# Performance work log

Hardware: AMD Instinct MI355X
Metric: run time of the kernel (lower is better)

Reference implementation:

```python
import jax, jax.numpy as jnp
import numpy as np

N_NODES = 50000
N_EDGES = 800000
IN_DIM, HID_DIM, OUT_DIM = 128, 64, 64


def spmm(row, col, val, dense):
    # sparse [N,N] (COO) @ dense [N,D] -> [N,D]
    gathered = dense[col] * val[:, None]          # [E, D]
    return jax.ops.segment_sum(gathered, row, num_segments=N_NODES)


def setup_inputs() -> dict:
    key = jax.random.key(0)
    ks = jax.random.split(key, 8)
    stdv1 = 1.0 / np.sqrt(HID_DIM)
    stdv2 = 1.0 / np.sqrt(OUT_DIM)
    return {
        "x": jax.random.normal(ks[0], (N_NODES, IN_DIM), dtype=jnp.float32),
        "edge_row": jax.random.randint(ks[1], (N_EDGES,), 0, N_NODES, dtype=jnp.int32),
        "edge_col": jax.random.randint(ks[2], (N_EDGES,), 0, N_NODES, dtype=jnp.int32),
        "edge_val": jax.random.uniform(ks[3], (N_EDGES,), dtype=jnp.float32),
        "W1": jax.random.uniform(ks[4], (IN_DIM, HID_DIM), jnp.float32, -stdv1, stdv1),
        "b1": jax.random.uniform(ks[5], (HID_DIM,), jnp.float32, -stdv1, stdv1),
        "W2": jax.random.uniform(ks[6], (HID_DIM, OUT_DIM), jnp.float32, -stdv2, stdv2),
        "b2": jax.random.uniform(ks[7], (OUT_DIM,), jnp.float32, -stdv2, stdv2),
    }


def reference(x, edge_row, edge_col, edge_val, W1, b1, W2, b2):
    # layer 1: support = x @ W1; out = adj @ support + b1; relu
    h = jax.nn.relu(spmm(edge_row, edge_col, edge_val, x @ W1) + b1)
    # dropout: eval mode (training=False) -> identity
    # layer 2
    return spmm(edge_row, edge_col, edge_val, h @ W2) + b2
```

## Files before the change

### kernel.cpp

```cpp
#include <hip/hip_runtime.h>


#define N_NODES 50000
#define N_EDGES 800000
#define IN_DIM  128
#define HID_DIM 64
#define OUT_DIM 64

#define RB   256
#define NB   ((N_NODES + RB - 1) / RB)
#define EPB  1024
#define NBLK_E ((N_EDGES + EPB - 1) / EPB)
#define BCAP 5120
#define GEMM_GRID ((N_NODES + 31) / 32)

typedef __attribute__((ext_vector_type(8))) short bf16x8;
typedef __attribute__((ext_vector_type(4))) float f32x4;

__device__ inline unsigned short f2bf(float x) {
    unsigned u = __float_as_uint(x);
    return (unsigned short)((u + 0x7FFFu + ((u >> 16) & 1u)) >> 16);
}
__device__ inline float bf2f(unsigned v) {
    return __uint_as_float(v << 16);
}

__global__ __launch_bounds__(256) void k_prep(
    const float* __restrict__ W1, unsigned short* __restrict__ Wt1,
    const float* __restrict__ W2, unsigned short* __restrict__ Wt2,
    int* __restrict__ bcur)
{
    int b = blockIdx.x, t = threadIdx.x;
    if (b < 32) {
        int e = b * 256 + t;
        int c = e / IN_DIM, k = e % IN_DIM;
        Wt1[c * IN_DIM + k] = f2bf(W1[k * HID_DIM + c]);
    } else if (b < 48) {
        int e2 = (b - 32) * 256 + t;
        int c = e2 / HID_DIM, k = e2 % HID_DIM;
        Wt2[c * HID_DIM + k] = f2bf(W2[k * OUT_DIM + c]);
    } else {
        if (t < NB) bcur[t] = 0;
    }
}

__global__ __launch_bounds__(256) void k_bscatter(
    const int* __restrict__ erow, const int* __restrict__ ecol,
    const float* __restrict__ eval_, int* __restrict__ bcur,
    uint2* __restrict__ bucketed)
{
    __shared__ uint2 sbuf[EPB];
    __shared__ int lc[NB];
    __shared__ int scr[256];
    __shared__ int lbase[NB];
    int t = threadIdx.x;
    if (t < NB) lc[t] = 0;
    __syncthreads();
    int base = blockIdx.x * EPB;
    int ne = min(EPB, N_EDGES - base);
    int bkt[4], rnk[4];
    unsigned w0v[4], vv[4];
    #pragma unroll
    for (int i = 0; i < 4; ++i) {
        int e = base + i * 256 + t;
        bkt[i] = -1;
        if (e < N_EDGES) {
            unsigned r = (unsigned)erow[e];
            bkt[i] = (int)(r >> 8);
            w0v[i] = (unsigned)ecol[e] | ((r & 255u) << 16) | ((r >> 8) << 24);
            vv[i] = __float_as_uint(eval_[e]);
            rnk[i] = atomicAdd(&lc[bkt[i]], 1);
        }
    }
    __syncthreads();
    int cnt = (t < NB) ? lc[t] : 0;
    scr[t] = cnt;
    __syncthreads();
    #pragma unroll
    for (int off = 1; off < 256; off <<= 1) {
        int add = (t >= off) ? scr[t - off] : 0;
        __syncthreads();
        scr[t] += add;
        __syncthreads();
    }
    int excl = scr[t] - cnt;
    __syncthreads();
    scr[t] = excl;
    if (t < NB) lbase[t] = cnt ? atomicAdd(&bcur[t], cnt) : 0;
    __syncthreads();
    #pragma unroll
    for (int i = 0; i < 4; ++i)
        if (bkt[i] >= 0)
            sbuf[scr[bkt[i]] + rnk[i]] = make_uint2(w0v[i], vv[i]);
    __syncthreads();
    #pragma unroll
    for (int i = 0; i < 4; ++i) {
        int idx = i * 256 + t;
        if (idx < ne) {
            uint2 p = sbuf[idx];
            int bk = (int)(p.x >> 24);
            bucketed[(size_t)bk * BCAP + lbase[bk] + (idx - scr[bk])] = p;
        }
    }
}

__global__ __launch_bounds__(256) void k_bfinal(
    const int* __restrict__ bcur, const uint2* __restrict__ bucketed,
    uint2* __restrict__ pairs, int2* __restrict__ offs2)
{
    __shared__ uint2 ebuf[BCAP];
    __shared__ int rcnt[256];
    __shared__ int rsc[256];
    int t = threadIdx.x, b = blockIdx.x;
    int ne = bcur[b];
    int base0 = b * BCAP;
    rcnt[t] = 0;
    __syncthreads();
    for (int i = t; i < ne; i += 256) {
        uint2 p = bucketed[(size_t)base0 + i];
        ebuf[i] = p;
        atomicAdd(&rcnt[(p.x >> 16) & 255], 1);
    }
    __syncthreads();
    int v = rcnt[t];
    rsc[t] = v;
    __syncthreads();
    #pragma unroll
    for (int off = 1; off < 256; off <<= 1) {
        int add = (t >= off) ? rsc[t - off] : 0;
        __syncthreads();
        rsc[t] += add;
        __syncthreads();
    }
    int start = base0 + rsc[t] - v;
    int gr = (b << 8) + t;
    if (gr < N_NODES) offs2[gr] = make_int2(start, start + v);
    rcnt[t] = start;
    __syncthreads();
    for (int i = t; i < ne; i += 256) {
        uint2 p = ebuf[i];
        int pos = atomicAdd(&rcnt[(p.x >> 16) & 255], 1);
        pairs[pos] = make_uint2(p.x & 0xFFFFu, p.y);
    }
}

template <int K, bool IN_BF16>
__device__ __forceinline__ void gemm_body(
    unsigned short* __restrict__ Al, unsigned short* __restrict__ Bl,
    const void* __restrict__ Xv, const unsigned short* __restrict__ Wt,
    unsigned short* __restrict__ out, int bid, int t)
{
    int m0 = bid * 32;
    #pragma unroll
    for (int i = 0; i < K / 32; ++i) {
        int u4 = i * 256 + t;
        int col = (u4 * 8) / K, k = (u4 * 8) % K;
        uint4 w = ((const uint4*)Wt)[u4];
        int byte = (col * K + k) * 2;
        byte ^= ((col & 7) << 4);
        *(uint4*)((char*)Bl + byte) = w;
    }
    if (IN_BF16) {
        const unsigned short* X = (const unsigned short*)Xv;
        int row = t / (K / 8), k = (t % (K / 8)) * 8;
        int grow = m0 + row;
        uint4 v = make_uint4(0, 0, 0, 0);
        if (grow < N_NODES)
            v = *(const uint4*)(X + (size_t)grow * K + k);
        int byte = (row * K + k) * 2;
        byte ^= ((row & 7) << 4);
        *(uint4*)((char*)Al + byte) = v;
    } else {
        const float* X = (const float*)Xv;
        #pragma unroll
        for (int i = 0; i < K / 64; ++i) {
            int f8 = i * 256 + t;
            int row = (f8 * 8) / K, k = (f8 * 8) % K;
            int grow = m0 + row;
            float4 xa = make_float4(0.f, 0.f, 0.f, 0.f), xb = xa;
            if (grow < N_NODES) {
                const float4* src = (const float4*)(X + (size_t)grow * K + k);
                xa = src[0];
                xb = src[1];
            }
            uint4 v;
            v.x = (unsigned)f2bf(xa.x) | ((unsigned)f2bf(xa.y) << 16);
            v.y = (unsigned)f2bf(xa.z) | ((unsigned)f2bf(xa.w) << 16);
            v.z = (unsigned)f2bf(xb.x) | ((unsigned)f2bf(xb.y) << 16);
            v.w = (unsigned)f2bf(xb.z) | ((unsigned)f2bf(xb.w) << 16);
            int byte = (row * K + k) * 2;
            byte ^= ((row & 7) << 4);
            *(uint4*)((char*)Al + byte) = v;
        }
    }
    __syncthreads();

    int w = t >> 6, l = t & 63;
    int lr0 = (w & 1) * 16;
    int c0  = (w >> 1) * 32;
    int lrow = lr0 + (l & 15);
    int kb = (l >> 4) * 8;
    int col0 = c0 + (l & 15), col1 = col0 + 16;
    f32x4 acc0 = {0.f, 0.f, 0.f, 0.f}, acc1 = {0.f, 0.f, 0.f, 0.f};
    #pragma unroll
    for (int kc = 0; kc < K / 32; ++kc) {
        int ka = kc * 32 + kb;
        int ab = (lrow * K + ka) * 2;  ab ^= ((lrow & 7) << 4);
        int bb0 = (col0 * K + ka) * 2; bb0 ^= ((col0 & 7) << 4);
        int bb1 = (col1 * K + ka) * 2; bb1 ^= ((col1 & 7) << 4);
        bf16x8 a  = *(const bf16x8*)((const char*)Al + ab);
        bf16x8 b0 = *(const bf16x8*)((const char*)Bl + bb0);
        bf16x8 b1 = *(const bf16x8*)((const char*)Bl + bb1);
        acc0 = __builtin_amdgcn_mfma_f32_16x16x32_bf16(a, b0, acc0, 0, 0, 0);
        acc1 = __builtin_amdgcn_mfma_f32_16x16x32_bf16(a, b1, acc1, 0, 0, 0);
    }
    int grow0 = m0 + lr0 + (l >> 4) * 4;
    #pragma unroll
    for (int j = 0; j < 4; ++j) {
        int gr = grow0 + j;
        if (gr < N_NODES) {
            out[(size_t)gr * 64 + col0] = f2bf(acc0[j]);
            out[(size_t)gr * 64 + col1] = f2bf(acc1[j]);
        }
    }
}

__global__ __launch_bounds__(256) void k_gemm1(
    const float* __restrict__ X, const unsigned short* __restrict__ Wt,
    unsigned short* __restrict__ out)
{
    __shared__ unsigned short Al[32 * IN_DIM];
    __shared__ unsigned short Bl[64 * IN_DIM];
    gemm_body<IN_DIM, false>(Al, Bl, X, Wt, out, blockIdx.x, threadIdx.x);
}

__global__ __launch_bounds__(512) void k_gather_gemm1(
    const int2* __restrict__ offs2, const uint2* __restrict__ pairs,
    const unsigned short* __restrict__ dense, const float* __restrict__ b1,
    const unsigned short* __restrict__ Wt2, unsigned short* __restrict__ out)
{
    __shared__ unsigned short Al[32 * 64];
    __shared__ unsigned short Bl[64 * 64];
    int t = threadIdx.x;
    int m0 = blockIdx.x * 32;
    {
        int u4 = t;
        int col = (u4 * 8) / 64, k = (u4 * 8) % 64;
        uint4 wv = ((const uint4*)Wt2)[u4];
        int byte = (col * 64 + k) * 2;
        byte ^= ((col & 7) << 4);
        *(uint4*)((char*)Bl + byte) = wv;
    }
    int w = t >> 6, d = t & 63;
    #pragma unroll 1
    for (int j = 0; j < 4; ++j) {
        int lr = w * 4 + j;
        int r = __builtin_amdgcn_readfirstlane(m0 + lr);
        float acc = 0.f;
        if (r < N_NODES) {
            int2 oe = offs2[r];
            int e0 = oe.x, e1 = oe.y;
            float a[8];
            a[0] = b1[d];
            #pragma unroll
            for (int i = 1; i < 8; ++i) a[i] = 0.f;
            int e = e0;
            for (; e + 8 <= e1; e += 8) {
                uint2 p[8];
                #pragma unroll
                for (int i = 0; i < 8; ++i) p[i] = pairs[e + i];
                unsigned v[8];
                #pragma unroll
                for (int i = 0; i < 8; ++i) v[i] = dense[(size_t)p[i].x * 64u + d];
                #pragma unroll
                for (int i = 0; i < 8; ++i)
                    a[i] = fmaf(__uint_as_float(p[i].y), bf2f(v[i]), a[i]);
            }
            if (e + 4 <= e1) {
                uint2 p[4];
                #pragma unroll
                for (int i = 0; i < 4; ++i) p[i] = pairs[e + i];
                unsigned v[4];
                #pragma unroll
                for (int i = 0; i < 4; ++i) v[i] = dense[(size_t)p[i].x * 64u + d];
                #pragma unroll
                for (int i = 0; i < 4; ++i)
                    a[i] = fmaf(__uint_as_float(p[i].y), bf2f(v[i]), a[i]);
                e += 4;
            }
            for (; e < e1; ++e) {
                uint2 p = pairs[e];
                a[0] = fmaf(__uint_as_float(p.y),
                            bf2f(dense[(size_t)p.x * 64u + d]), a[0]);
            }
            acc = ((a[0] + a[1]) + (a[2] + a[3])) +
                  ((a[4] + a[5]) + (a[6] + a[7]));
            acc = fmaxf(acc, 0.f);
        }
        int byte = (lr * 64 + d) * 2;
        byte ^= ((lr & 7) << 4);
        *(unsigned short*)((char*)Al + byte) = f2bf(acc);
    }
    __syncthreads();
    int l = t & 63;
    int lr0 = (w & 1) * 16;
    int c0  = (w >> 1) * 16;
    int lrow = lr0 + (l & 15);
    int kb = (l >> 4) * 8;
    int col = c0 + (l & 15);
    f32x4 acc0 = {0.f, 0.f, 0.f, 0.f};
    #pragma unroll
    for (int kc = 0; kc < 2; ++kc) {
        int ka = kc * 32 + kb;
        int ab = (lrow * 64 + ka) * 2; ab ^= ((lrow & 7) << 4);
        int bb = (col * 64 + ka) * 2;  bb ^= ((col & 7) << 4);
        bf16x8 a = *(const bf16x8*)((const char*)Al + ab);
        bf16x8 b = *(const bf16x8*)((const char*)Bl + bb);
        acc0 = __builtin_amdgcn_mfma_f32_16x16x32_bf16(a, b, acc0, 0, 0, 0);
    }
    int grow0 = m0 + lr0 + (l >> 4) * 4;
    #pragma unroll
    for (int j = 0; j < 4; ++j) {
        int gr = grow0 + j;
        if (gr < N_NODES)
            out[(size_t)gr * 64 + col] = f2bf(acc0[j]);
    }
}

__global__ __launch_bounds__(256) void k_gather2(
    const int2* __restrict__ offs2, const uint2* __restrict__ pairs,
    const unsigned short* __restrict__ dense, const float* __restrict__ bias,
    float* __restrict__ outp)
{
    int t = threadIdx.x;
    int r = __builtin_amdgcn_readfirstlane(blockIdx.x * 4 + (t >> 6));
    int d = t & 63;
    int2 oe = offs2[r];
    int e0 = oe.x, e1 = oe.y;
    float a[8];
    a[0] = bias[d];
    #pragma unroll
    for (int i = 1; i < 8; ++i) a[i] = 0.f;
    int e = e0;
    for (; e + 8 <= e1; e += 8) {
        uint2 p[8];
        #pragma unroll
        for (int i = 0; i < 8; ++i) p[i] = pairs[e + i];
        unsigned v[8];
        #pragma unroll
        for (int i = 0; i < 8; ++i) v[i] = dense[(size_t)p[i].x * 64u + d];
        #pragma unroll
        for (int i = 0; i < 8; ++i)
            a[i] = fmaf(__uint_as_float(p[i].y), bf2f(v[i]), a[i]);
    }
    if (e + 4 <= e1) {
        uint2 p[4];
        #pragma unroll
        for (int i = 0; i < 4; ++i) p[i] = pairs[e + i];
        unsigned v[4];
        #pragma unroll
        for (int i = 0; i < 4; ++i) v[i] = dense[(size_t)p[i].x * 64u + d];
        #pragma unroll
        for (int i = 0; i < 4; ++i)
            a[i] = fmaf(__uint_as_float(p[i].y), bf2f(v[i]), a[i]);
        e += 4;
    }
    for (; e < e1; ++e) {
        uint2 p = pairs[e];
        a[0] = fmaf(__uint_as_float(p.y),
                    bf2f(dense[(size_t)p.x * 64u + d]), a[0]);
    }
    float acc = ((a[0] + a[1]) + (a[2] + a[3])) +
                ((a[4] + a[5]) + (a[6] + a[7]));
    outp[(size_t)r * 64 + d] = acc;
}

extern "C" void kernel_launch(void* const* d_in, const int* in_sizes, int n_in,
                              void* d_out, int out_size, void* d_ws, size_t ws_size,
                              hipStream_t stream)
{
    const float* x     = (const float*)d_in[0];
    const int*   erow  = (const int*)d_in[1];
    const int*   ecol  = (const int*)d_in[2];
    const float* eval_ = (const float*)d_in[3];
    const float* W1    = (const float*)d_in[4];
    const float* b1    = (const float*)d_in[5];
    const float* W2    = (const float*)d_in[6];
    const float* b2    = (const float*)d_in[7];
    float* out = (float*)d_out;

    uint2* pairs    = (uint2*)d_ws;
    uint2* bucketed = pairs + (size_t)NB * BCAP;
    unsigned short* support = (unsigned short*)(bucketed + (size_t)NB * BCAP);
    unsigned short* Wt1 = support + (size_t)N_NODES * 64;
    unsigned short* Wt2 = Wt1 + IN_DIM * HID_DIM;
    int*  bcur  = (int*)(Wt2 + HID_DIM * OUT_DIM);
    int2* offs2 = (int2*)(bcur + NB);

    unsigned short* support2 = (unsigned short*)(offs2 + N_NODES + 2);

    const int row_grid = N_NODES / 4;

    k_prep<<<49, 256, 0, stream>>>(W1, Wt1, W2, Wt2, bcur);
    k_bscatter<<<NBLK_E, 256, 0, stream>>>(erow, ecol, eval_, bcur, bucketed);
    k_bfinal<<<NB, 256, 0, stream>>>(bcur, bucketed, pairs, offs2);
    k_gemm1<<<GEMM_GRID, 256, 0, stream>>>(x, Wt1, support);
    k_gather_gemm1<<<GEMM_GRID, 512, 0, stream>>>(
        offs2, pairs, support, b1, Wt2, support2);
    k_gather2<<<row_grid, 256, 0, stream>>>(
        offs2, pairs, support2, b2, out);
}
```

Before: 96.68 us.

## Fuse bucket scatter with first GEMM, split bucket finalize, deepen gather unroll

Bucket scatter and the x@W1 GEMM now run as one launch, with block ranges assigned to each role and a shared LDS buffer, so the two independent stages overlap and one launch disappears. Bucket finalization is split into two blocks per bucket, each handling half the rows with a wave-level shuffle scan. It rereads the bucket from global memory instead of staging it in a 40KB LDS buffer, which should raise occupancy and parallelism at the cost of a second read. The layer-2 gather is unrolled to 16 edges per iteration for more memory-level parallelism, which raises register use.

```diff
diff --git a/kernel.cpp b/kernel.cpp
--- a/kernel.cpp
+++ b/kernel.cpp
@@ -41,106 +41,6 @@
         Wt2[c * HID_DIM + k] = f2bf(W2[k * OUT_DIM + c]);
     } else {
         if (t < NB) bcur[t] = 0;
-    }
-}
-
-__global__ __launch_bounds__(256) void k_bscatter(
-    const int* __restrict__ erow, const int* __restrict__ ecol,
-    const float* __restrict__ eval_, int* __restrict__ bcur,
-    uint2* __restrict__ bucketed)
-{
-    __shared__ uint2 sbuf[EPB];
-    __shared__ int lc[NB];
-    __shared__ int scr[256];
-    __shared__ int lbase[NB];
-    int t = threadIdx.x;
-    if (t < NB) lc[t] = 0;
-    __syncthreads();
-    int base = blockIdx.x * EPB;
-    int ne = min(EPB, N_EDGES - base);
-    int bkt[4], rnk[4];
-    unsigned w0v[4], vv[4];
-    #pragma unroll
-    for (int i = 0; i < 4; ++i) {
-        int e = base + i * 256 + t;
-        bkt[i] = -1;
-        if (e < N_EDGES) {
-            unsigned r = (unsigned)erow[e];
-            bkt[i] = (int)(r >> 8);
-            w0v[i] = (unsigned)ecol[e] | ((r & 255u) << 16) | ((r >> 8) << 24);
-            vv[i] = __float_as_uint(eval_[e]);
-            rnk[i] = atomicAdd(&lc[bkt[i]], 1);
-        }
-    }
-    __syncthreads();
-    int cnt = (t < NB) ? lc[t] : 0;
-    scr[t] = cnt;
-    __syncthreads();
-    #pragma unroll
-    for (int off = 1; off < 256; off <<= 1) {
-        int add = (t >= off) ? scr[t - off] : 0;
-        __syncthreads();
-        scr[t] += add;
-        __syncthreads();
-    }
-    int excl = scr[t] - cnt;
-    __syncthreads();
-    scr[t] = excl;
-    if (t < NB) lbase[t] = cnt ? atomicAdd(&bcur[t], cnt) : 0;
-    __syncthreads();
-    #pragma unroll
-    for (int i = 0; i < 4; ++i)
-        if (bkt[i] >= 0)
-            sbuf[scr[bkt[i]] + rnk[i]] = make_uint2(w0v[i], vv[i]);
-    __syncthreads();
-    #pragma unroll
-    for (int i = 0; i < 4; ++i) {
-        int idx = i * 256 + t;
-        if (idx < ne) {
-            uint2 p = sbuf[idx];
-            int bk = (int)(p.x >> 24);
-            bucketed[(size_t)bk * BCAP + lbase[bk] + (idx - scr[bk])] = p;
-        }
-    }
-}
-
-__global__ __launch_bounds__(256) void k_bfinal(
-    const int* __restrict__ bcur, const uint2* __restrict__ bucketed,
-    uint2* __restrict__ pairs, int2* __restrict__ offs2)
-{
-    __shared__ uint2 ebuf[BCAP];
-    __shared__ int rcnt[256];
-    __shared__ int rsc[256];
-    int t = threadIdx.x, b = blockIdx.x;
-    int ne = bcur[b];
-    int base0 = b * BCAP;
-    rcnt[t] = 0;
-    __syncthreads();
-    for (int i = t; i < ne; i += 256) {
-        uint2 p = bucketed[(size_t)base0 + i];
-        ebuf[i] = p;
-        atomicAdd(&rcnt[(p.x >> 16) & 255], 1);
-    }
-    __syncthreads();
-    int v = rcnt[t];
-    rsc[t] = v;
-    __syncthreads();
-    #pragma unroll
-    for (int off = 1; off < 256; off <<= 1) {
-        int add = (t >= off) ? rsc[t - off] : 0;
-        __syncthreads();
-        rsc[t] += add;
-        __syncthreads();
-    }
-    int start = base0 + rsc[t] - v;
-    int gr = (b << 8) + t;
-    if (gr < N_NODES) offs2[gr] = make_int2(start, start + v);
-    rcnt[t] = start;
-    __syncthreads();
-    for (int i = t; i < ne; i += 256) {
-        uint2 p = ebuf[i];
-        int pos = atomicAdd(&rcnt[(p.x >> 16) & 255], 1);
-        pairs[pos] = make_uint2(p.x & 0xFFFFu, p.y);
     }
 }
 
@@ -225,13 +125,125 @@
     }
 }
 
-__global__ __launch_bounds__(256) void k_gemm1(
-    const float* __restrict__ X, const unsigned short* __restrict__ Wt,
-    unsigned short* __restrict__ out)
-{
-    __shared__ unsigned short Al[32 * IN_DIM];
-    __shared__ unsigned short Bl[64 * IN_DIM];
-    gemm_body<IN_DIM, false>(Al, Bl, X, Wt, out, blockIdx.x, threadIdx.x);
+__global__ __launch_bounds__(256) void k_mega(
+    const int* __restrict__ erow, const int* __restrict__ ecol,
+    const float* __restrict__ eval_, int* __restrict__ bcur,
+    uint2* __restrict__ bucketed,
+    const float* __restrict__ X, const unsigned short* __restrict__ Wt1,
+    unsigned short* __restrict__ support)
+{
+    __shared__ __align__(16) unsigned char smem[24576];
+    int t = threadIdx.x;
+    if (blockIdx.x >= NBLK_E) {
+        gemm_body<IN_DIM, false>((unsigned short*)smem,
+                                 (unsigned short*)(smem + 8192),
+                                 X, Wt1, support, blockIdx.x - NBLK_E, t);
+        return;
+    }
+    uint2* sbuf  = (uint2*)smem;
+    int*   lc    = (int*)(smem + 8192);
+    int*   scr   = lc + 256;
+    int*   lbase = scr + 256;
+    if (t < NB) lc[t] = 0;
+    __syncthreads();
+    int base = blockIdx.x * EPB;
+    int ne = min(EPB, N_EDGES - base);
+    int bkt[4], rnk[4];
+    unsigned w0v[4], vv[4];
+    #pragma unroll
+    for (int i = 0; i < 4; ++i) {
+        int e = base + i * 256 + t;
+        bkt[i] = -1;
+        if (e < N_EDGES) {
+            unsigned r = (unsigned)erow[e];
+            bkt[i] = (int)(r >> 8);
+            w0v[i] = (unsigned)ecol[e] | ((r & 255u) << 16) | ((r >> 8) << 24);
+            vv[i] = __float_as_uint(eval_[e]);
+            rnk[i] = atomicAdd(&lc[bkt[i]], 1);
+        }
+    }
+    __syncthreads();
+    int cnt = (t < NB) ? lc[t] : 0;
+    scr[t] = cnt;
+    __syncthreads();
+    #pragma unroll
+    for (int off = 1; off < 256; off <<= 1) {
+        int add = (t >= off) ? scr[t - off] : 0;
+        __syncthreads();
+        scr[t] += add;
+        __syncthreads();
+    }
+    int excl = scr[t] - cnt;
+    __syncthreads();
+    scr[t] = excl;
+    if (t < NB) lbase[t] = cnt ? atomicAdd(&bcur[t], cnt) : 0;
+    __syncthreads();
+    #pragma unroll
+    for (int i = 0; i < 4; ++i)
+        if (bkt[i] >= 0)
+            sbuf[scr[bkt[i]] + rnk[i]] = make_uint2(w0v[i], vv[i]);
+    __syncthreads();
+    #pragma unroll
+    for (int i = 0; i < 4; ++i) {
+        int idx = i * 256 + t;
+        if (idx < ne) {
+            uint2 p = sbuf[idx];
+            int bk = (int)(p.x >> 24);
+            bucketed[(size_t)bk * BCAP + lbase[bk] + (idx - scr[bk])] = p;
+        }
+    }
+}
+
+__global__ __launch_bounds__(256) void k_bfinal2(
+    const int* __restrict__ bcur, const uint2* __restrict__ bucketed,
+    uint2* __restrict__ pairs, int2* __restrict__ offs2)
+{
+    __shared__ int rcnt[128], rst[128];
+    __shared__ int nkept_sh;
+    int t = threadIdx.x, blk = blockIdx.x;
+    int B = blk >> 1, h = blk & 1;
+    int ne = bcur[B];
+    size_t eb = (size_t)B * BCAP;
+    if (t < 128) rcnt[t] = 0;
+    __syncthreads();
+    for (int i = t; i < ne; i += 256) {
+        unsigned w0 = bucketed[eb + i].x;
+        int rl = (int)((w0 >> 16) & 255u);
+        if ((rl >> 7) == h) atomicAdd(&rcnt[rl & 127], 1);
+    }
+    __syncthreads();
+    if (t < 64) {
+        int c0 = rcnt[2 * t], c1 = rcnt[2 * t + 1];
+        int s = c0 + c1, inc = s;
+        #pragma unroll
+        for (int off = 1; off < 64; off <<= 1) {
+            int o = __shfl_up(inc, off, 64);
+            if (t >= off) inc += o;
+        }
+        int excl = inc - s;
+        int tot = __shfl(inc, 63, 64);
+        if (t == 0) nkept_sh = tot;
+        rst[2 * t] = excl;
+        rst[2 * t + 1] = excl + c0;
+    }
+    __syncthreads();
+    int nk = nkept_sh;
+    int regionBase = (int)eb + (h ? (ne - nk) : 0);
+    if (t < 128) {
+        int gr = B * 256 + h * 128 + t;
+        int st = regionBase + rst[t];
+        if (gr < N_NODES) offs2[gr] = make_int2(st, st + rcnt[t]);
+        rst[t] = st;
+    }
+    __syncthreads();
+    for (int i = t; i < ne; i += 256) {
+        uint2 p = bucketed[eb + i];
+        int rl = (int)((p.x >> 16) & 255u);
+        if ((rl >> 7) == h) {
+            int pos = atomicAdd(&rst[rl & 127], 1);
+            pairs[pos] = make_uint2(p.x & 0xFFFFu, p.y);
+        }
+    }
 }
 
 __global__ __launch_bounds__(512) void k_gather_gemm1(
@@ -337,12 +349,23 @@
     int d = t & 63;
     int2 oe = offs2[r];
     int e0 = oe.x, e1 = oe.y;
-    float a[8];
+    float a[16];
     a[0] = bias[d];
     #pragma unroll
-    for (int i = 1; i < 8; ++i) a[i] = 0.f;
+    for (int i = 1; i < 16; ++i) a[i] = 0.f;
     int e = e0;
-    for (; e + 8 <= e1; e += 8) {
+    for (; e + 16 <= e1; e += 16) {
+        uint2 p[16];
+        #pragma unroll
+        for (int i = 0; i < 16; ++i) p[i] = pairs[e + i];
+        unsigned v[16];
+        #pragma unroll
+        for (int i = 0; i < 16; ++i) v[i] = dense[(size_t)p[i].x * 64u + d];
+        #pragma unroll
+        for (int i = 0; i < 16; ++i)
+            a[i] = fmaf(__uint_as_float(p[i].y), bf2f(v[i]), a[i]);
+    }
+    if (e + 8 <= e1) {
         uint2 p[8];
         #pragma unroll
         for (int i = 0; i < 8; ++i) p[i] = pairs[e + i];
@@ -352,6 +375,7 @@
         #pragma unroll
         for (int i = 0; i < 8; ++i)
             a[i] = fmaf(__uint_as_float(p[i].y), bf2f(v[i]), a[i]);
+        e += 8;
     }
     if (e + 4 <= e1) {
         uint2 p[4];
@@ -370,9 +394,11 @@
         a[0] = fmaf(__uint_as_float(p.y),
                     bf2f(dense[(size_t)p.x * 64u + d]), a[0]);
     }
-    float acc = ((a[0] + a[1]) + (a[2] + a[3])) +
-                ((a[4] + a[5]) + (a[6] + a[7]));
-    outp[(size_t)r * 64 + d] = acc;
+    float s0 = ((a[0] + a[1]) + (a[2] + a[3])) +
+               ((a[4] + a[5]) + (a[6] + a[7]));
+    float s1 = ((a[8] + a[9]) + (a[10] + a[11])) +
+               ((a[12] + a[13]) + (a[14] + a[15]));
+    outp[(size_t)r * 64 + d] = s0 + s1;
 }
 
 extern "C" void kernel_launch(void* const* d_in, const int* in_sizes, int n_in,
@@ -396,15 +422,14 @@
     unsigned short* Wt2 = Wt1 + IN_DIM * HID_DIM;
     int*  bcur  = (int*)(Wt2 + HID_DIM * OUT_DIM);
     int2* offs2 = (int2*)(bcur + NB);
-
     unsigned short* support2 = (unsigned short*)(offs2 + N_NODES + 2);
 
     const int row_grid = N_NODES / 4;
 
     k_prep<<<49, 256, 0, stream>>>(W1, Wt1, W2, Wt2, bcur);
-    k_bscatter<<<NBLK_E, 256, 0, stream>>>(erow, ecol, eval_, bcur, bucketed);
-    k_bfinal<<<NB, 256, 0, stream>>>(bcur, bucketed, pairs, offs2);
-    k_gemm1<<<GEMM_GRID, 256, 0, stream>>>(x, Wt1, support);
+    k_mega<<<NBLK_E + GEMM_GRID, 256, 0, stream>>>(
+        erow, ecol, eval_, bcur, bucketed, x, Wt1, support);
+    k_bfinal2<<<2 * NB, 256, 0, stream>>>(bcur, bucketed, pairs, offs2);
     k_gather_gemm1<<<GEMM_GRID, 512, 0, stream>>>(
         offs2, pairs, support, b1, Wt2, support2);
     k_gather2<<<row_grid, 256, 0, stream>>>(
```

Result: faster. 94.74 us (-2.0%).
